# Optimization experiments

Measured on AMD Instinct MI355X. Metric: run time of the kernel, lower is better.

The kernel has to match this reference:

```python
import jax, jax.numpy as jnp
import numpy as np

MARGIN = 0.3
NORM = 2.0  # p-norm used by both pairwise() and PairwiseDistance

M, C = 65536, 256   # n*h*w pixels, feature channels
K, P, Q = 20, 2048, 2048  # classes 1..nclass-1, positives, negatives per class


def setup_inputs() -> dict:
    key = jax.random.key(0)
    k1, k2, k3 = jax.random.split(key, 3)
    features = jax.random.normal(k1, (M, C), dtype=jnp.float32)
    pos_idx = jax.random.randint(k2, (K, P), 0, M)
    neg_idx = jax.random.randint(k3, (K, Q), 0, M)
    return {"features": features, "pos_idx": pos_idx, "neg_idx": neg_idx}


def _pairwise(x, y):
    # torch: clamp(xx - 2xy + yy, 0); (dis + eps) ** (1/norm)
    eps = 0.0001 / x.shape[1]
    xx = jnp.sum(x * x, axis=1)           # [P]
    yy = jnp.sum(y * y, axis=1)           # [Q]
    xy = x @ y.T                           # [P,Q] GEMM
    dis = jnp.clip(xx[:, None] - 2.0 * xy + yy[None, :], 0.0)
    return (dis + eps) ** (1.0 / NORM)


def _pdist(x1, x2):
    # PairwiseDistance: (clamp(sum(|x1-x2|^p), 0) + eps) ** (1/p)
    eps = 0.0001 / x1.shape[1]
    out = jnp.sum(jnp.abs(x1 - x2) ** NORM, axis=1)
    return (jnp.clip(out, 0.0) + eps) ** (1.0 / NORM)


def _class_loss(pos, neg):
    # hard mining on detached features (indices only, as in generate_triplet_simple)
    pos_d = jax.lax.stop_gradient(pos)
    neg_d = jax.lax.stop_gradient(neg)
    hp = jnp.argmax(_pairwise(pos_d, pos_d), axis=1)   # hardest positive per anchor
    hn = jnp.argmin(_pairwise(pos_d, neg_d), axis=1)   # hardest negative per anchor
    d_p = _pdist(pos, pos[hp])
    d_n = _pdist(pos, neg[hn])
    return jnp.mean(jnp.clip(MARGIN + d_p - d_n, 0.0))


def reference(features, pos_idx, neg_idx):
    f = jax.nn.sigmoid(features)          # torch.sigmoid(features)
    pos = f[pos_idx]                      # [K,P,C]
    neg = f[neg_idx]                      # [K,Q,C]
    losses = jax.vmap(_class_loss)(pos, neg)  # per-class triplet losses
    return jnp.sum(losses)                # loss accumulated over classes
```

## Files before the change

### kernel.cpp

```cpp
#include <hip/hip_runtime.h>
#include <stdint.h>

#define M_ROWS 65536
#define C_DIM  256
#define K_CLS  20
#define P_POS  2048
#define MARGIN_F 0.3f
#define EPS_D (0.0001f / 256.0f)
#define SCALE1 0x7F7F7F7Fu

typedef float floatx4 __attribute__((ext_vector_type(4)));
typedef int   intx8   __attribute__((ext_vector_type(8)));
union Frag8 { intx8 v; uint4 q[2]; };

__device__ __forceinline__ void async_copy16(const void* g, void* l) {
    __builtin_amdgcn_global_load_lds(
        (const __attribute__((address_space(1))) void*)g,
        (__attribute__((address_space(3))) void*)l, 16, 0, 0);
}
__device__ __forceinline__ float sigm(float x) { return 1.f / (1.f + __expf(-x)); }

__global__ __launch_bounds__(256) void sigmoid_norm_k(
        const float* __restrict__ feat,
        unsigned int* __restrict__ S8,
        float* __restrict__ xx,
        unsigned int* __restrict__ hp,
        unsigned int* __restrict__ hn) {
    {
        const int idx = blockIdx.x * 256 + threadIdx.x;
        if (idx < K_CLS * P_POS) { hp[idx] = 0u; hn[idx] = 0xFFFFFFFFu; }
    }
    const int wave = threadIdx.x >> 6, lane = threadIdx.x & 63;
    const int row = blockIdx.x * 4 + wave;
    const float4 v = *(const float4*)(feat + (size_t)row * C_DIM + lane * 4);

    const int p01 = __builtin_amdgcn_cvt_pk_fp8_f32(sigm(v.x), sigm(v.y), 0, false);
    const int p23 = __builtin_amdgcn_cvt_pk_fp8_f32(sigm(v.z), sigm(v.w), 0, false);
    const unsigned int packed = (unsigned int)(p01 & 0xFFFF) | ((unsigned int)p23 << 16);
    S8[(size_t)row * 64 + lane] = packed;

    const float q0 = __builtin_amdgcn_cvt_f32_fp8(p01, 0);
    const float q1 = __builtin_amdgcn_cvt_f32_fp8(p01, 1);
    const float q2 = __builtin_amdgcn_cvt_f32_fp8(p23, 0);
    const float q3 = __builtin_amdgcn_cvt_f32_fp8(p23, 1);
    float sum = q0 * q0 + q1 * q1 + q2 * q2 + q3 * q3;
#pragma unroll
    for (int off = 32; off; off >>= 1) sum += __shfl_down(sum, off);
    if (lane == 0) xx[row] = sum;
}

__global__ __launch_bounds__(256, 3) void select_k(
        const unsigned int* __restrict__ S8,
        const float* __restrict__ xx,
        const int* __restrict__ pos_idx,
        const int* __restrict__ neg_idx,
        unsigned int* __restrict__ hp,
        unsigned int* __restrict__ hn) {
    __shared__ __align__(16) unsigned char Bt[2][32 * 256];

    const int tid    = threadIdx.x;
    const int w      = tid >> 6;
    const int lane   = tid & 63;
    const int lane15 = lane & 15;
    const int quad   = lane >> 4;

    const int bid    = blockIdx.x;
    const int ctid   = bid % 40;
    const int rest   = bid / 40;
    const int i_blk  = rest >> 2;
    const int jq     = rest & 3;
    const int k      = ctid >> 1;
    const int isNeg  = ctid & 1;
    const int i0     = i_blk * 256;
    const int j0     = jq * 512;

    const int* __restrict__ idxA = pos_idx + k * P_POS;
    const int* __restrict__ idxB = (isNeg ? neg_idx : pos_idx) + k * P_POS;
    unsigned int* outKey         = (isNeg ? hn : hp) + k * P_POS;

    const char* S8B = (const char*)S8;

    const int rl  = lane >> 4;
    const int cch = lane & 15;
    int rloc[2], soff[2];
#pragma unroll
    for (int c = 0; c < 2; ++c) {
        rloc[c] = (w * 2 + c) * 4 + rl;
        soff[c] = (cch ^ (rloc[c] & 15)) << 4;
    }

    int g_st[2];
#pragma unroll
    for (int c = 0; c < 2; ++c) g_st[c] = idxB[j0 + rloc[c]];
#pragma unroll
    for (int c = 0; c < 2; ++c)
        async_copy16(S8B + ((size_t)(uint32_t)g_st[c] << 8) + soff[c],
                     (char*)&Bt[0][0] + (w * 2 + c) * 1024);
#pragma unroll
    for (int c = 0; c < 2; ++c) g_st[c] = idxB[j0 + 32 + rloc[c]];

    float yv0 = xx[idxB[j0 + lane15]];
    float yv1 = xx[idxB[j0 + 16 + lane15]];
    int idx_n0 = idxB[j0 + 32 + lane15];
    int idx_n1 = idxB[j0 + 48 + lane15];

    Frag8 A_reg[4][2];
#pragma unroll
    for (int si = 0; si < 4; ++si) {
        const int gi = idxA[i0 + w * 64 + si * 16 + lane15];
        const char* rb = S8B + ((size_t)(uint32_t)gi << 8) + quad * 32;
#pragma unroll
        for (int s = 0; s < 2; ++s) {
            A_reg[si][s].q[0] = *(const uint4*)(rb + s * 128);
            A_reg[si][s].q[1] = *(const uint4*)(rb + s * 128 + 16);
        }
    }

    int blo[2], bhi[2];
#pragma unroll
    for (int s = 0; s < 2; ++s) {
        const int c0 = s * 8 + quad * 2;
        blo[s] = lane15 * 256 + ((c0 ^ lane15) << 4);
        bhi[s] = lane15 * 256 + (((c0 + 1) ^ lane15) << 4);
    }

    float bestv[16];
    const float binit = isNeg ? 3.4e38f : -3.4e38f;
#pragma unroll
    for (int t = 0; t < 16; ++t) bestv[t] = binit;

#pragma unroll 2
    for (int jc = 0; jc < 16; ++jc) {
        __syncthreads();

        const float nv0 = xx[idx_n0];
        const float nv1 = xx[idx_n1];

        if (jc < 15) {
            char* lb = (char*)(&Bt[(jc + 1) & 1][0]);
#pragma unroll
            for (int c = 0; c < 2; ++c)
                async_copy16(S8B + ((size_t)(uint32_t)g_st[c] << 8) + soff[c],
                             lb + (w * 2 + c) * 1024);
        }
        {
            const int nt = j0 + (jc < 14 ? jc + 2 : 15) * 32;
#pragma unroll
            for (int c = 0; c < 2; ++c) g_st[c] = idxB[nt + rloc[c]];
            idx_n0 = idxB[nt + lane15];
            idx_n1 = idxB[nt + 16 + lane15];
        }

        const char* Bb = (const char*)(&Bt[jc & 1][0]);
        floatx4 acc[2][4];
#pragma unroll
        for (int ct = 0; ct < 2; ++ct)
#pragma unroll
            for (int si = 0; si < 4; ++si)
                acc[ct][si] = (floatx4){0.f, 0.f, 0.f, 0.f};

#pragma unroll
        for (int s = 0; s < 2; ++s) {
            Frag8 bf0, bf1;
            bf0.q[0] = *(const uint4*)(Bb + blo[s]);
            bf0.q[1] = *(const uint4*)(Bb + bhi[s]);
            bf1.q[0] = *(const uint4*)(Bb + blo[s] + 4096);
            bf1.q[1] = *(const uint4*)(Bb + bhi[s] + 4096);
#pragma unroll
            for (int si = 0; si < 4; ++si)
                acc[0][si] = __builtin_amdgcn_mfma_scale_f32_16x16x128_f8f6f4(
                    A_reg[si][s].v, bf0.v, acc[0][si], 0, 0,
                    0, SCALE1, 0, SCALE1);
#pragma unroll
            for (int si = 0; si < 4; ++si)
                acc[1][si] = __builtin_amdgcn_mfma_scale_f32_16x16x128_f8f6f4(
                    A_reg[si][s].v, bf1.v, acc[1][si], 0, 0,
                    0, SCALE1, 0, SCALE1);
        }

        const uint32_t jb0 = (uint32_t)((j0 + (jc << 5)) | lane15);
        const uint32_t jb1 = jb0 | 16u;
#pragma unroll
        for (int ct = 0; ct < 2; ++ct) {
            const float yv = ct ? yv1 : yv0;
            const uint32_t jb = ct ? jb1 : jb0;
#pragma unroll
            for (int si = 0; si < 4; ++si)
#pragma unroll
                for (int r = 0; r < 4; ++r) {
                    const float g = fmaf(-2.f, acc[ct][si][r], yv);
                    const float enc = __uint_as_float(
                        (__float_as_uint(g) & 0xFFFFF800u) | jb);
                    const int slot = si * 4 + r;
                    bestv[slot] = isNeg ? fminf(bestv[slot], enc)
                                        : fmaxf(bestv[slot], enc);
                }
        }
        yv0 = nv0; yv1 = nv1;
    }

#pragma unroll
    for (int slot = 0; slot < 16; ++slot) {
#pragma unroll
        for (int off = 1; off < 16; off <<= 1) {
            const float ov = __shfl_xor(bestv[slot], off);
            bestv[slot] = isNeg ? fminf(bestv[slot], ov) : fmaxf(bestv[slot], ov);
        }
    }
    if (lane15 == 0) {
#pragma unroll
        for (int si = 0; si < 4; ++si)
#pragma unroll
            for (int r = 0; r < 4; ++r) {
                const int row = w * 64 + si * 16 + quad * 4 + r;
                const uint32_t u = __float_as_uint(bestv[si * 4 + r]);
                const uint32_t key = (u & 0x80000000u) ? ~u : (u | 0x80000000u);
                if (isNeg) atomicMin(&outKey[i0 + row], key);
                else       atomicMax(&outKey[i0 + row], key);
            }
    }
}

#define ACC16(UA, UP, UN)                                                     \
    {                                                                         \
        float xa, d;                                                          \
        xa = __builtin_amdgcn_cvt_f32_fp8((int)(UA), 0);                      \
        d = xa - __builtin_amdgcn_cvt_f32_fp8((int)(UP), 0); dp += d * d;     \
        d = xa - __builtin_amdgcn_cvt_f32_fp8((int)(UN), 0); dn += d * d;     \
        xa = __builtin_amdgcn_cvt_f32_fp8((int)(UA), 1);                      \
        d = xa - __builtin_amdgcn_cvt_f32_fp8((int)(UP), 1); dp += d * d;     \
        d = xa - __builtin_amdgcn_cvt_f32_fp8((int)(UN), 1); dn += d * d;     \
        xa = __builtin_amdgcn_cvt_f32_fp8((int)(UA), 2);                      \
        d = xa - __builtin_amdgcn_cvt_f32_fp8((int)(UP), 2); dp += d * d;     \
        d = xa - __builtin_amdgcn_cvt_f32_fp8((int)(UN), 2); dn += d * d;     \
        xa = __builtin_amdgcn_cvt_f32_fp8((int)(UA), 3);                      \
        d = xa - __builtin_amdgcn_cvt_f32_fp8((int)(UP), 3); dp += d * d;     \
        d = xa - __builtin_amdgcn_cvt_f32_fp8((int)(UN), 3); dn += d * d;     \
    }

__global__ __launch_bounds__(256) void loss_k(
        const unsigned int* __restrict__ S8,
        const int* __restrict__ pos_idx,
        const int* __restrict__ neg_idx,
        const unsigned int* __restrict__ hp,
        const unsigned int* __restrict__ hn,
        float* __restrict__ terms) {
    const int tid    = threadIdx.x;
    const int lane15 = tid & 15;
    const int grp    = tid >> 4;
    const int a      = blockIdx.x * 16 + grp;
    const int k      = a >> 11;
    const int i      = a & 2047;
    const int* pidx = pos_idx + (k << 11);
    const int* nidx = neg_idx + (k << 11);
    const unsigned int kp = hp[a], kn = hn[a];
    const int jp = (int)((kp & 0x80000000u) ? (kp & 2047u) : ((~kp) & 2047u));
    const int jn = (int)((kn & 0x80000000u) ? (kn & 2047u) : ((~kn) & 2047u));
    const int ga = pidx[i];
    const int gp = pidx[jp];
    const int gn = nidx[jn];

    const char* S8B = (const char*)S8;
    const uint4 va = *(const uint4*)(S8B + ((size_t)(uint32_t)ga << 8) + lane15 * 16);
    const uint4 vp = *(const uint4*)(S8B + ((size_t)(uint32_t)gp << 8) + lane15 * 16);
    const uint4 vn = *(const uint4*)(S8B + ((size_t)(uint32_t)gn << 8) + lane15 * 16);

    float dp = 0.f, dn = 0.f;
    ACC16(va.x, vp.x, vn.x)
    ACC16(va.y, vp.y, vn.y)
    ACC16(va.z, vp.z, vn.z)
    ACC16(va.w, vp.w, vn.w)

#pragma unroll
    for (int off = 1; off < 16; off <<= 1) {
        dp += __shfl_xor(dp, off);
        dn += __shfl_xor(dn, off);
    }
    if (lane15 == 0) {
        const float d_p = sqrtf(fmaxf(dp, 0.f) + EPS_D);
        const float d_n = sqrtf(fmaxf(dn, 0.f) + EPS_D);
        terms[a] = fmaxf(MARGIN_F + d_p - d_n, 0.f);
    }
}

__global__ __launch_bounds__(1024) void reduce_k(
        const float* __restrict__ terms, float* __restrict__ out) {
    __shared__ float red[1024];
    float s = 0.f;
    for (int i = threadIdx.x; i < K_CLS * P_POS; i += 1024) s += terms[i];
    red[threadIdx.x] = s;
    __syncthreads();
    for (int off = 512; off; off >>= 1) {
        if ((int)threadIdx.x < off) red[threadIdx.x] += red[threadIdx.x + off];
        __syncthreads();
    }
    if (threadIdx.x == 0) out[0] = red[0] * (1.0f / (float)P_POS);
}

extern "C" void kernel_launch(void* const* d_in, const int* in_sizes, int n_in,
                              void* d_out, int out_size, void* d_ws, size_t ws_size,
                              hipStream_t stream) {
    const float* feat    = (const float*)d_in[0];
    const int*   pos_idx = (const int*)d_in[1];
    const int*   neg_idx = (const int*)d_in[2];

    char* ws = (char*)d_ws;
    unsigned int* S8 = (unsigned int*)ws;
    float*        xx = (float*)(ws + 16777216);
    unsigned int* hp = (unsigned int*)(ws + 17039360);
    unsigned int* hn = (unsigned int*)(ws + 17203200);
    float*     terms = (float*)(ws + 17367040);

    sigmoid_norm_k<<<M_ROWS / 4, 256, 0, stream>>>(feat, S8, xx, hp, hn);

    select_k<<<32 * 40, 256, 0, stream>>>(S8, xx, pos_idx, neg_idx, hp, hn);

    loss_k<<<(K_CLS * P_POS) / 16, 256, 0, stream>>>(S8, pos_idx, neg_idx, hp, hn, terms);

    reduce_k<<<1, 1024, 0, stream>>>(terms, (float*)d_out);
}
```

Before: 181.4 us.

## Load B fragments directly into registers, dropping LDS staging and block barriers

Each wave now gathers its own B-operand fp8 rows straight from global memory into registers, with a one-step register prefetch, instead of async-copying shared tiles into double-buffered LDS and synchronising the block. This removes LDS traffic and __syncthreads stalls. Because every wave re-gathers the same B rows, global and L2 traffic rises fourfold, and launch bounds drop to 2 waves per SIMD to make room for the extra prefetch registers, which lowers occupancy.

Measured after the change: 212.5 us. +17.1%, slower.

```diff
diff --git a/kernel.cpp b/kernel.cpp
--- a/kernel.cpp
+++ b/kernel.cpp
@@ -13,11 +13,6 @@
 typedef int   intx8   __attribute__((ext_vector_type(8)));
 union Frag8 { intx8 v; uint4 q[2]; };
 
-__device__ __forceinline__ void async_copy16(const void* g, void* l) {
-    __builtin_amdgcn_global_load_lds(
-        (const __attribute__((address_space(1))) void*)g,
-        (__attribute__((address_space(3))) void*)l, 16, 0, 0);
-}
 __device__ __forceinline__ float sigm(float x) { return 1.f / (1.f + __expf(-x)); }
 
 __global__ __launch_bounds__(256) void sigmoid_norm_k(
@@ -49,15 +44,13 @@
     if (lane == 0) xx[row] = sum;
 }
 
-__global__ __launch_bounds__(256, 3) void select_k(
+__global__ __launch_bounds__(256, 2) void select_k(
         const unsigned int* __restrict__ S8,
         const float* __restrict__ xx,
         const int* __restrict__ pos_idx,
         const int* __restrict__ neg_idx,
         unsigned int* __restrict__ hp,
         unsigned int* __restrict__ hn) {
-    __shared__ __align__(16) unsigned char Bt[2][32 * 256];
-
     const int tid    = threadIdx.x;
     const int w      = tid >> 6;
     const int lane   = tid & 63;
@@ -80,30 +73,6 @@
 
     const char* S8B = (const char*)S8;
 
-    const int rl  = lane >> 4;
-    const int cch = lane & 15;
-    int rloc[2], soff[2];
-#pragma unroll
-    for (int c = 0; c < 2; ++c) {
-        rloc[c] = (w * 2 + c) * 4 + rl;
-        soff[c] = (cch ^ (rloc[c] & 15)) << 4;
-    }
-
-    int g_st[2];
-#pragma unroll
-    for (int c = 0; c < 2; ++c) g_st[c] = idxB[j0 + rloc[c]];
-#pragma unroll
-    for (int c = 0; c < 2; ++c)
-        async_copy16(S8B + ((size_t)(uint32_t)g_st[c] << 8) + soff[c],
-                     (char*)&Bt[0][0] + (w * 2 + c) * 1024);
-#pragma unroll
-    for (int c = 0; c < 2; ++c) g_st[c] = idxB[j0 + 32 + rloc[c]];
-
-    float yv0 = xx[idxB[j0 + lane15]];
-    float yv1 = xx[idxB[j0 + 16 + lane15]];
-    int idx_n0 = idxB[j0 + 32 + lane15];
-    int idx_n1 = idxB[j0 + 48 + lane15];
-
     Frag8 A_reg[4][2];
 #pragma unroll
     for (int si = 0; si < 4; ++si) {
@@ -116,13 +85,24 @@
         }
     }
 
-    int blo[2], bhi[2];
-#pragma unroll
-    for (int s = 0; s < 2; ++s) {
-        const int c0 = s * 8 + quad * 2;
-        blo[s] = lane15 * 256 + ((c0 ^ lane15) << 4);
-        bhi[s] = lane15 * 256 + (((c0 + 1) ^ lane15) << 4);
-    }
+    int i_c0 = idxB[j0 + lane15];
+    int i_c1 = idxB[j0 + 16 + lane15];
+    float yv0 = xx[i_c0];
+    float yv1 = xx[i_c1];
+    Frag8 cur[2][2];
+    {
+        const char* b0 = S8B + ((size_t)(uint32_t)i_c0 << 8) + quad * 32;
+        const char* b1 = S8B + ((size_t)(uint32_t)i_c1 << 8) + quad * 32;
+#pragma unroll
+        for (int s = 0; s < 2; ++s) {
+            cur[0][s].q[0] = *(const uint4*)(b0 + s * 128);
+            cur[0][s].q[1] = *(const uint4*)(b0 + s * 128 + 16);
+            cur[1][s].q[0] = *(const uint4*)(b1 + s * 128);
+            cur[1][s].q[1] = *(const uint4*)(b1 + s * 128 + 16);
+        }
+    }
+    int idx_n0 = idxB[j0 + 32 + lane15];
+    int idx_n1 = idxB[j0 + 48 + lane15];
 
     float bestv[16];
     const float binit = isNeg ? 3.4e38f : -3.4e38f;
@@ -131,27 +111,24 @@
 
 #pragma unroll 2
     for (int jc = 0; jc < 16; ++jc) {
-        __syncthreads();
-
+        Frag8 nb[2][2];
+        const char* b0 = S8B + ((size_t)(uint32_t)idx_n0 << 8) + quad * 32;
+        const char* b1 = S8B + ((size_t)(uint32_t)idx_n1 << 8) + quad * 32;
+#pragma unroll
+        for (int s = 0; s < 2; ++s) {
+            nb[0][s].q[0] = *(const uint4*)(b0 + s * 128);
+            nb[0][s].q[1] = *(const uint4*)(b0 + s * 128 + 16);
+            nb[1][s].q[0] = *(const uint4*)(b1 + s * 128);
+            nb[1][s].q[1] = *(const uint4*)(b1 + s * 128 + 16);
+        }
         const float nv0 = xx[idx_n0];
         const float nv1 = xx[idx_n1];
-
-        if (jc < 15) {
-            char* lb = (char*)(&Bt[(jc + 1) & 1][0]);
-#pragma unroll
-            for (int c = 0; c < 2; ++c)
-                async_copy16(S8B + ((size_t)(uint32_t)g_st[c] << 8) + soff[c],
-                             lb + (w * 2 + c) * 1024);
-        }
         {
             const int nt = j0 + (jc < 14 ? jc + 2 : 15) * 32;
-#pragma unroll
-            for (int c = 0; c < 2; ++c) g_st[c] = idxB[nt + rloc[c]];
             idx_n0 = idxB[nt + lane15];
             idx_n1 = idxB[nt + 16 + lane15];
         }
 
-        const char* Bb = (const char*)(&Bt[jc & 1][0]);
         floatx4 acc[2][4];
 #pragma unroll
         for (int ct = 0; ct < 2; ++ct)
@@ -161,20 +138,15 @@
 
 #pragma unroll
         for (int s = 0; s < 2; ++s) {
-            Frag8 bf0, bf1;
-            bf0.q[0] = *(const uint4*)(Bb + blo[s]);
-            bf0.q[1] = *(const uint4*)(Bb + bhi[s]);
-            bf1.q[0] = *(const uint4*)(Bb + blo[s] + 4096);
-            bf1.q[1] = *(const uint4*)(Bb + bhi[s] + 4096);
 #pragma unroll
             for (int si = 0; si < 4; ++si)
                 acc[0][si] = __builtin_amdgcn_mfma_scale_f32_16x16x128_f8f6f4(
-                    A_reg[si][s].v, bf0.v, acc[0][si], 0, 0,
+                    A_reg[si][s].v, cur[0][s].v, acc[0][si], 0, 0,
                     0, SCALE1, 0, SCALE1);
 #pragma unroll
             for (int si = 0; si < 4; ++si)
                 acc[1][si] = __builtin_amdgcn_mfma_scale_f32_16x16x128_f8f6f4(
-                    A_reg[si][s].v, bf1.v, acc[1][si], 0, 0,
+                    A_reg[si][s].v, cur[1][s].v, acc[1][si], 0, 0,
                     0, SCALE1, 0, SCALE1);
         }
 
@@ -196,6 +168,11 @@
                                         : fmaxf(bestv[slot], enc);
                 }
         }
+
+#pragma unroll
+        for (int ct = 0; ct < 2; ++ct)
+#pragma unroll
+            for (int s = 0; s < 2; ++s) cur[ct][s] = nb[ct][s];
         yv0 = nv0; yv1 = nv1;
     }
 
```
